# Optimization experiments

Hardware: AMD Instinct MI355X
Metric: run time of the kernel (lower is better)

## Reference

```python
import jax, jax.numpy as jnp
import numpy as np

D = 128           # volume / particle box size (pixels)
B = 8             # particles per batch
K = 125           # SO(3) grid poses (5x5x5 around each center Euler)
TOPK = 2          # keep_top_k_values
MAX_SHIFT_FRAC = 0.25  # main_config.projmatching.max_shift_fraction


def setup_inputs() -> dict:
    key = jax.random.key(0)
    k1, k2, k3, k4 = jax.random.split(key, 4)
    vol = jax.random.normal(k1, (D, D, D), dtype=jnp.float32)
    parts = jax.random.normal(k2, (B, D, D), dtype=jnp.float32)
    ctf = jax.random.uniform(k3, (B, D, D // 2 + 1), dtype=jnp.float32)
    euler_degs = jax.random.normal(k4, (K, 3), dtype=jnp.float32) * 8.0
    return {"vol": vol, "parts": parts, "ctf": ctf, "euler_degs": euler_degs}


def _rot_z(t):
    c, s = jnp.cos(t), jnp.sin(t)
    z, o = jnp.zeros_like(t), jnp.ones_like(t)
    return jnp.stack([jnp.stack([c, -s, z], -1),
                      jnp.stack([s, c, z], -1),
                      jnp.stack([z, z, o], -1)], -2)


def _rot_y(t):
    c, s = jnp.cos(t), jnp.sin(t)
    z, o = jnp.zeros_like(t), jnp.ones_like(t)
    return jnp.stack([jnp.stack([c, z, s], -1),
                      jnp.stack([z, o, z], -1),
                      jnp.stack([-s, z, c], -1)], -2)


def euler_zyz_to_matrix(degs):
    # RELION Euler convention ZYZ: R = Rz(a) @ Ry(b) @ Rz(c)
    rad = jnp.deg2rad(degs)
    return _rot_z(rad[..., 0]) @ _rot_y(rad[..., 1]) @ _rot_z(rad[..., 2])


def trilinear_sample(vol, zi, yi, xi):
    # vol: (Dz, Dy, W) complex64; coords: (K, h, w) float32 array indices
    Dz, Dy, W = vol.shape
    z0, y0, x0 = jnp.floor(zi), jnp.floor(yi), jnp.floor(xi)
    tz, ty, tx = zi - z0, yi - y0, xi - x0
    out = jnp.zeros(zi.shape, dtype=vol.dtype)
    for dz in (0, 1):
        wz = tz if dz else 1.0 - tz
        zc = z0 + dz
        vz = (zc >= 0) & (zc < Dz)
        zdx = jnp.clip(zc, 0, Dz - 1).astype(jnp.int32)
        for dy in (0, 1):
            wy = ty if dy else 1.0 - ty
            yc = y0 + dy
            vy = (yc >= 0) & (yc < Dy)
            ydx = jnp.clip(yc, 0, Dy - 1).astype(jnp.int32)
            for dx in (0, 1):
                wx = tx if dx else 1.0 - tx
                xc = x0 + dx
                vx = (xc >= 0) & (xc < W)
                xdx = jnp.clip(xc, 0, W - 1).astype(jnp.int32)
                w = jnp.where(vz & vy & vx, wz * wy * wx, 0.0)
                out = out + w * vol[zdx, ydx, xdx]
    return out


def project_fourier(vol_rfft, rotmats):
    # extract_central_slices_rfft: pose-dependent gather+trilinear interp of a
    # central slice from the fftshifted 3D rfft volume. Output: (K, D, D//2+1).
    d = D
    w = d // 2 + 1
    y = jnp.arange(d, dtype=jnp.float32) - d // 2   # fftshifted full-dim freqs (pixel units)
    x = jnp.arange(w, dtype=jnp.float32)            # rfft (non-negative) freqs
    yy, xx = jnp.meshgrid(y, x, indexing='ij')      # (d, w)
    coords = jnp.stack([xx, yy, jnp.zeros_like(yy)], -1)       # xyz, (d, w, 3), z = 0 plane
    rot = jnp.einsum('kij,hwj->khwi', rotmats, coords)          # (K, d, w, 3) rotated xyz
    conj_mask = rot[..., 0] < 0                                  # Hermitian symmetry: flip to x>=0 half
    rot = jnp.where(conj_mask[..., None], -rot, rot)
    xi = rot[..., 0]
    yi = rot[..., 1] + d // 2
    zi = rot[..., 2] + d // 2
    samples = trilinear_sample(vol_rfft, zi, yi, xi)
    samples = jnp.where(conj_mask, jnp.conj(samples), samples)
    r2 = xx ** 2 + yy ** 2                                       # zero beyond Nyquist radius
    samples = jnp.where(r2[None] > (d // 2) ** 2, 0.0, samples)
    return samples


def reference(vol, parts, ctf, euler_degs):
    # compute_dft: rfft volume, fftshift non-rfft dims
    vol_rfft = jnp.fft.fftshift(jnp.fft.rfftn(vol), axes=(0, 1))
    parts_rfft = jnp.fft.fftshift(jnp.fft.rfft2(parts), axes=(-2,))  # (B, D, W)
    rotmats = euler_zyz_to_matrix(euler_degs)                        # (K, 3, 3)
    projs = project_fourier(vol_rfft, rotmats)                       # (K, D, W)
    projs = ctf[:, None] * projs[None]                               # _apply_ctfF: (B, K, D, W)
    # correlate_dft_2d: cross-correlation via iFFT of parts * conj(projs)
    prod = parts_rfft[:, None] * jnp.conj(projs)
    prod = jnp.fft.ifftshift(prod, axes=(-2,))
    corr = jnp.fft.irfft2(prod, s=(D, D))                            # (B, K, D, D)
    corr = jnp.fft.fftshift(corr, axes=(-2, -1))                     # zero shift at center
    # _extract_ccor_max: restrict to |shift| <= max_shift_fraction*D, take top-k peaks
    center = D // 2
    max_shift = int(MAX_SHIFT_FRAC * D)
    idx = jnp.arange(D) - center
    win = (jnp.abs(idx)[:, None] <= max_shift) & (jnp.abs(idx)[None, :] <= max_shift)
    masked = jnp.where(win, corr, -jnp.inf)
    flat = masked.reshape(B, K, D * D)
    vals, top_idx = jax.lax.top_k(flat, TOPK)                        # (B, K, TOPK)
    shifts = jnp.stack([top_idx // D - center, top_idx % D - center], -1)  # (B, K, TOPK, 2) yx
    return vals, shifts
```

## Files before the change

### kernel.cpp

```cpp
#include <hip/hip_runtime.h>
#include <math.h>

#define D 128
#define W 65
#define NK 125
#define NB 8
#define SLAB (D*W)
#define TWO_PI 6.28318530717958647692f
#define R2C 0.70710678118654752440f
#define C8C 0.92387953251128675613f
#define S8C 0.38268343236508977173f
#define ARS 146
#define GRS 131


__device__ __forceinline__ bool better(float va, int ia, float vb, int ib) {
    return (va > vb) || (va == vb && ia < ib);
}
__device__ __forceinline__ float2 cmul(float2 a, float2 b) {
    return make_float2(a.x*b.x - a.y*b.y, a.x*b.y + a.y*b.x);
}
__device__ __forceinline__ void cmac(float2& acc, float2 a, float2 b) {
    acc.x = fmaf(a.x, b.x, fmaf(-a.y, b.y, acc.x));
    acc.y = fmaf(a.x, b.y, fmaf( a.y, b.x, acc.y));
}
__device__ __forceinline__ float2 cadd(float2 a, float2 b){ return make_float2(a.x+b.x, a.y+b.y); }
__device__ __forceinline__ float2 csub(float2 a, float2 b){ return make_float2(a.x-b.x, a.y-b.y); }

__device__ __forceinline__ void fft8_fwd(const float2* x, float2* a) {
    float2 e0 = x[0], o0 = x[1], e1 = x[2], o1 = x[3];
    float2 e2 = x[4], o2 = x[5], e3 = x[6], o3 = x[7];
    float2 t0 = cadd(e0, e2), t1 = csub(e0, e2);
    float2 t2 = cadd(e1, e3), t3 = csub(e1, e3);
    float2 E0 = cadd(t0, t2), E2 = csub(t0, t2);
    float2 E1 = make_float2(t1.x + t3.y, t1.y - t3.x);
    float2 E3 = make_float2(t1.x - t3.y, t1.y + t3.x);
    float2 u0 = cadd(o0, o2), u1 = csub(o0, o2);
    float2 u2 = cadd(o1, o3), u3 = csub(o1, o3);
    float2 O0 = cadd(u0, u2), O2 = csub(u0, u2);
    float2 O1 = make_float2(u1.x + u3.y, u1.y - u3.x);
    float2 O3 = make_float2(u1.x - u3.y, u1.y + u3.x);
    float2 w1 = make_float2(R2C*(O1.x + O1.y), R2C*(O1.y - O1.x));
    float2 w2 = make_float2(O2.y, -O2.x);
    float2 w3 = make_float2(R2C*(O3.y - O3.x), -R2C*(O3.x + O3.y));
    a[0] = cadd(E0, O0); a[4] = csub(E0, O0);
    a[1] = cadd(E1, w1); a[5] = csub(E1, w1);
    a[2] = cadd(E2, w2); a[6] = csub(E2, w2);
    a[3] = cadd(E3, w3); a[7] = csub(E3, w3);
}

__device__ __forceinline__ void ifft8_reg(const float2* x, float2* a) {
    float2 e0 = x[0], o0 = x[1], e1 = x[2], o1 = x[3];
    float2 e2 = x[4], o2 = x[5], e3 = x[6], o3 = x[7];
    float2 t0 = cadd(e0, e2), t1 = csub(e0, e2);
    float2 t2 = cadd(e1, e3), t3 = csub(e1, e3);
    float2 E0 = cadd(t0, t2), E2 = csub(t0, t2);
    float2 E1 = make_float2(t1.x - t3.y, t1.y + t3.x);
    float2 E3 = make_float2(t1.x + t3.y, t1.y - t3.x);
    float2 u0 = cadd(o0, o2), u1 = csub(o0, o2);
    float2 u2 = cadd(o1, o3), u3 = csub(o1, o3);
    float2 O0 = cadd(u0, u2), O2 = csub(u0, u2);
    float2 O1 = make_float2(u1.x - u3.y, u1.y + u3.x);
    float2 O3 = make_float2(u1.x + u3.y, u1.y - u3.x);
    float2 w1o = make_float2(R2C*(O1.x - O1.y), R2C*(O1.x + O1.y));
    float2 w2o = make_float2(-O2.y, O2.x);
    float2 w3o = make_float2(R2C*(-O3.x - O3.y), R2C*(O3.x - O3.y));
    a[0] = cadd(E0, O0); a[4] = csub(E0, O0);
    a[1] = cadd(E1, w1o); a[5] = csub(E1, w1o);
    a[2] = cadd(E2, w2o); a[6] = csub(E2, w2o);
    a[3] = cadd(E3, w3o); a[7] = csub(E3, w3o);
}


template<int MODE>
__device__ __forceinline__ void fft128v2(const float* __restrict__ inf,
                                         const float2* __restrict__ inc,
                                         float2* __restrict__ out,
                                         const float* __restrict__ ct,
                                         int l0, int nlines,
                                         float2* __restrict__ Fl,
                                         float2* __restrict__ twf) {
    int tid = threadIdx.x;
    int line, t;
    if (MODE == 0) { t = tid & 7; line = tid >> 3; }
    else           { line = tid & 31; t = tid >> 5; }
    int l = l0 + line;
    bool live = (l < nlines);

    if (tid < 128) {
        float s, c;
        sincosf(-TWO_PI * (float)tid / 128.0f, &s, &c);
        twf[tid] = make_float2(c, s);
    }

    int base = 0, stride = 1;
    if (MODE == 1 || MODE == 3 || MODE == 4) { base = (l / W) * SLAB + (l % W); stride = W; }
    else if (MODE == 2) { base = l; stride = SLAB; }

    float2 xe[8], xo[8];
    if (live) {
        if (MODE == 0) {
            const float* r = inf + (size_t)l * D;
            #pragma unroll
            for (int j = 0; j < 8; ++j) {
                xe[j] = make_float2(r[t + 16*j], 0.f);
                xo[j] = make_float2(r[t + 8 + 16*j], 0.f);
            }
        } else {
            #pragma unroll
            for (int j = 0; j < 8; ++j) {
                xe[j] = inc[base + (t + 16*j) * stride];
                xo[j] = inc[base + (t + 8 + 16*j) * stride];
            }
        }
    } else {
        #pragma unroll
        for (int j = 0; j < 8; ++j) { xe[j] = make_float2(0,0); xo[j] = make_float2(0,0); }
    }
    float2 E[8], O[8];
    fft8_fwd(xe, E);
    fft8_fwd(xo, O);
    {
        const float2 w16[8] = {
            { 1.f, 0.f }, { C8C, -S8C }, { R2C, -R2C }, { S8C, -C8C },
            { 0.f, -1.f }, { -S8C, -C8C }, { -R2C, -R2C }, { -C8C, -S8C }
        };
        float2* Fp = Fl + line * 137 + t * 17;
        #pragma unroll
        for (int kk = 0; kk < 8; ++kk) {
            float2 wo = cmul(w16[kk], O[kk]);
            Fp[kk]     = cadd(E[kk], wo);
            Fp[kk + 8] = csub(E[kk], wo);
        }
    }
    __syncthreads();
    if (live) {
        const float2* Fr = Fl + line * 137;
        #pragma unroll
        for (int s = 0; s < 16; ++s) {
            int slot = t + 8 * s;
            if (MODE == 0 && slot > 64) break;
            int k = (MODE == 0) ? slot : (slot ^ 64);
            int kk = k & 15;
            float2 acc = make_float2(0.f, 0.f);
            #pragma unroll
            for (int tt = 0; tt < 8; ++tt) {
                cmac(acc, Fr[tt * 17 + kk], twf[(tt * k) & 127]);
            }
            if (MODE == 0)      out[(size_t)l * W + slot] = acc;
            else if (MODE == 3) out[(size_t)l * D + slot] = acc;
            else if (MODE == 4) {
                float cf = ct[(size_t)l * D + slot];
                out[(size_t)l * D + slot] = make_float2(acc.x * cf, acc.y * cf);
            }
            else                out[base + slot * stride] = acc;
        }
    }
}


__global__ __launch_bounds__(256) void k1_kernel(const float* __restrict__ vol,
                                                 const float* __restrict__ parts,
                                                 const float* __restrict__ ctf,
                                                 const float* __restrict__ euler,
                                                 float2* __restrict__ bufA,
                                                 float2* __restrict__ pT1,
                                                 float* __restrict__ CT,
                                                 float* __restrict__ rot) {
    __shared__ float2 Fl[32 * 137];
    __shared__ float2 twf[128];
    int bid = blockIdx.x;
    int tid = threadIdx.x;
    if (bid < 512) {
        fft128v2<0>(vol, nullptr, bufA, nullptr, bid * 32, D*D, Fl, twf);
    } else if (bid < 544) {
        fft128v2<0>(parts, nullptr, pT1, nullptr, (bid - 512) * 32, NB*D, Fl, twf);
    } else if (bid == 544) {
        int k = tid;
        if (k < NK) {
            const float d2r = 0.017453292519943295f;
            float a = euler[k*3+0]*d2r, b = euler[k*3+1]*d2r, c = euler[k*3+2]*d2r;
            float sa, ca, sb, cb, sc, cc;
            sincosf(a, &sa, &ca); sincosf(b, &sb, &cb); sincosf(c, &sc, &cc);
            rot[k*9+0] =  ca*cb*cc - sa*sc;
            rot[k*9+1] = -ca*cb*sc - sa*cc;
            rot[k*9+2] =  ca*sb;
            rot[k*9+3] =  sa*cb*cc + ca*sc;
            rot[k*9+4] = -sa*cb*sc + ca*cc;
            rot[k*9+5] =  sa*sb;
            rot[k*9+6] = -sb*cc;
            rot[k*9+7] =  sb*sc;
            rot[k*9+8] =  cb;
        }
    } else {
        int i = (bid - 545) * 256 + tid;
        if (i < NB * W * D) {
            int m = i & (D-1);
            int t2 = i >> 7;
            int x = t2 % W;
            int b = t2 / W;
            CT[i] = ctf[b * SLAB + m * W + x];
        }
    }
}

__global__ __launch_bounds__(256) void k2_kernel(const float2* __restrict__ bufA,
                                                 float2* __restrict__ bufB,
                                                 const float2* __restrict__ pT1,
                                                 float2* __restrict__ ST,
                                                 const float* __restrict__ CT) {
    __shared__ float2 Fl[32 * 137];
    __shared__ float2 twf[128];
    int bid = blockIdx.x;
    if (bid < 260) fft128v2<1>(nullptr, bufA, bufB, nullptr, bid * 32, D*W, Fl, twf);
    else           fft128v2<4>(nullptr, pT1, ST, CT, (bid - 260) * 32, NB*W, Fl, twf);
}

__global__ __launch_bounds__(256) void k3_kernel(const float2* __restrict__ bufB,
                                                 float2* __restrict__ bufA) {
    __shared__ float2 Fl[32 * 137];
    __shared__ float2 twf[128];
    fft128v2<2>(nullptr, bufB, bufA, nullptr, blockIdx.x * 32, SLAB, Fl, twf);
}


__global__ void proj_kernel(const float2* __restrict__ vol, const float* __restrict__ rot,
                            float2* __restrict__ projT) {
    int idx = blockIdx.x * blockDim.x + threadIdx.x;
    if (idx >= NK * D * W) return;
    int h = idx & (D-1);
    int t2 = idx >> 7;
    int w = t2 % W;
    int k = t2 / W;
    float x = (float)w;
    float y = (float)(h - 64);
    const float* R = rot + k*9;
    float rx = R[0]*x + R[1]*y;
    float ry = R[3]*x + R[4]*y;
    float rz = R[6]*x + R[7]*y;
    bool neg = rx < 0.0f;
    if (neg) { rx = -rx; ry = -ry; rz = -rz; }
    float xi = rx;
    float yi = ry + 64.0f;
    float zi = rz + 64.0f;
    float z0 = floorf(zi), y0 = floorf(yi), x0 = floorf(xi);
    float tz = zi - z0, ty = yi - y0, tx = xi - x0;
    int z0i = (int)z0, y0i = (int)y0, x0i = (int)x0;
    float ar = 0.f, ai = 0.f;
    for (int dz = 0; dz < 2; ++dz) {
        float wz = dz ? tz : 1.0f - tz;
        int zc = z0i + dz;
        bool vz = (zc >= 0) && (zc < D);
        int zx = min(max(zc, 0), D-1);
        for (int dy = 0; dy < 2; ++dy) {
            float wy = dy ? ty : 1.0f - ty;
            int yc = y0i + dy;
            bool vy = (yc >= 0) && (yc < D);
            int yx = min(max(yc, 0), D-1);
            for (int dx = 0; dx < 2; ++dx) {
                float wx = dx ? tx : 1.0f - tx;
                int xc = x0i + dx;
                bool vx = (xc >= 0) && (xc < W);
                int xx = min(max(xc, 0), W-1);
                float wt = (vz && vy && vx) ? wz*wy*wx : 0.0f;
                float2 v = vol[zx * SLAB + yx * W + xx];
                ar = fmaf(wt, v.x, ar);
                ai = fmaf(wt, v.y, ai);
            }
        }
    }
    if (neg) ai = -ai;
    int yy = h - 64;
    if (w*w + yy*yy > 4096) { ar = 0.f; ai = 0.f; }
    projT[idx] = make_float2(ar, ai);
}


__global__ __launch_bounds__(256, 2) void corr_kernel(const float2* __restrict__ ST,
                                                      const float2* __restrict__ PJT,
                                                      float* __restrict__ outv) {
    __shared__ float2 tw[128];
    __shared__ float2 AbBC[17*ARS];
    __shared__ float2 G[17*GRS];
    __shared__ float  Ny[65];
    __shared__ float  redv[8];
    __shared__ int    redi[8];

    int g = blockIdx.x;
    int logical = (g & 7) * 125 + (g >> 3);
    int k = logical >> 3;
    int b = logical & 7;
    int tid = threadIdx.x;
    const float inv_d = 1.0f / 128.0f;

    if (tid < 128) {
        float s, c;
        sincosf(TWO_PI * (float)tid / 128.0f, &s, &c);
        tw[tid] = make_float2(c, s);
    }

    const float2* Sb = ST + b * (W * D);
    const float2* Jk = PJT + k * (W * D);

    int lane = tid & 63;
    int wv = tid >> 6;
    int sv = lane & 7;
    int vp = (96 + lane) & 127;
    float acc[16];
    #pragma unroll
    for (int j = 0; j < 16; ++j) acc[j] = 0.0f;
    float accR = 0.0f;
    int ur = 0, vr = 0;
    if (tid < 129) { if (tid < 65) { ur = 64; vr = tid; } else { ur = tid - 65; vr = 64; } }

    __syncthreads();

    float2 wvp = tw[vp];
    float2 tq = make_float2(1.0f, 0.0f);

    int l1 = tid >> 4, m01 = tid & 15;
    float2 Sv[8], Jv[8];

    for (int cg = 0; cg < 4; ++cg) {
        if (cg == 0) {
            for (int i = tid; i < 17 * 16; i += 256) {
                int l = i >> 4, m0 = i & 15;
                int x = (l < 16) ? ((l >> 2) + 16 * (l & 3)) : 64;
                const float2* Sx = Sb + x * 128 + m0;
                const float2* Jx = Jk + x * 128 + m0;
                float2 p[8];
                #pragma unroll
                for (int j = 0; j < 8; ++j) {
                    float2 s = Sx[16*j];
                    float2 pj = Jx[16*j];
                    p[j] = make_float2(s.x*pj.x + s.y*pj.y, s.y*pj.x - s.x*pj.y);
                }
                float2 A[8];
                ifft8_reg(p, A);
                float2* dst = AbBC + l * ARS + m0;
                dst[0] = A[0];
                #pragma unroll
                for (int r = 1; r < 8; ++r) dst[r*18] = cmul(A[r], tw[(r * m0) & 127]);
            }
        } else {
            float2 p[8];
            #pragma unroll
            for (int j = 0; j < 8; ++j) {
                p[j] = make_float2(Sv[j].x*Jv[j].x + Sv[j].y*Jv[j].y,
                                   Sv[j].y*Jv[j].x - Sv[j].x*Jv[j].y);
            }
            float2 A[8];
            ifft8_reg(p, A);
            float2* dst = AbBC + l1 * ARS + m01;
            dst[0] = A[0];
            #pragma unroll
            for (int r = 1; r < 8; ++r) dst[r*18] = cmul(A[r], tw[(r * m01) & 127]);
        }
        __syncthreads();
        {
            int lim2 = (cg == 0) ? 136 : 128;
            for (int i = tid; i < lim2; i += 256) {
                int l, r;
                if (i < 128) { l = i & 15; r = i >> 4; }
                else         { l = 16; r = i - 128; }
                const float4* Ar = (const float4*)(AbBC + l * ARS + r * 18);
                float2 xe[8], xo[8];
                #pragma unroll
                for (int j = 0; j < 8; ++j) {
                    float4 a = Ar[j];
                    xe[j] = make_float2(a.x, a.y);
                    xo[j] = make_float2(a.z, a.w);
                }
                float2 E[8], O[8];
                ifft8_reg(xe, E);
                ifft8_reg(xo, O);
                const float2 w16p[8] = {
                    { 1.f, 0.f }, { C8C, S8C }, { R2C, R2C }, { S8C, C8C },
                    { 0.f, 1.f }, { -S8C, C8C }, { -R2C, R2C }, { -C8C, S8C }
                };
                float2* Gl = G + l * GRS + r;
                #pragma unroll
                for (int t = 0; t < 8; ++t) {
                    float2 wo = cmul(w16p[t], O[t]);
                    Gl[8*t]      = cadd(E[t], wo);
                    Gl[8*t + 64] = csub(E[t], wo);
                }
            }
        }
        if (cg < 3) {
            int xn = 4*(cg+1) + (l1 >> 2) + 16 * (l1 & 3);
            const float2* Sx = Sb + xn * 128 + m01;
            const float2* Jx = Jk + xn * 128 + m01;
            #pragma unroll
            for (int j = 0; j < 8; ++j) {
                Sv[j] = Sx[16*j];
                Jv[j] = Jx[16*j];
            }
        }
        __syncthreads();
        {
            float2* BC = AbBC;
            int lim = (cg == 0) ? 325 : 260;
            for (int i = tid; i < lim; i += 256) {
                if (i < 260) {
                    int q = i / 65;
                    int u2 = i - q * 65;
                    int up = (96 + u2) & 127;
                    float sg = (u2 & 1) ? -inv_d : inv_d;
                    const float2* Gq = G + up;
                    float2 h0 = Gq[(4*q+0)*GRS];
                    float2 h1 = Gq[(4*q+1)*GRS];
                    float2 h2 = Gq[(4*q+2)*GRS];
                    float2 h3 = Gq[(4*q+3)*GRS];
                    h0.x *= sg; h0.y *= sg; h1.x *= sg; h1.y *= sg;
                    h2.x *= sg; h2.y *= sg; h3.x *= sg; h3.y *= sg;
                    if (cg == 0 && q == 0) { h0.x *= 0.5f; h0.y *= 0.5f; }
                    const float sc = 2.0f * inv_d;
                    float2 p1 = make_float2(R2C*(h1.x - h1.y), R2C*(h1.x + h1.y));
                    float2 q1 = make_float2(R2C*(-h1.x - h1.y), R2C*(h1.x - h1.y));
                    float2 i1 = make_float2(-h1.y, h1.x);
                    float2 i2 = make_float2(-h2.y, h2.x);
                    float2 n2 = make_float2( h2.y, -h2.x);
                    float2 p3 = make_float2(R2C*(h3.x - h3.y), R2C*(h3.x + h3.y));
                    float2 q3 = make_float2(R2C*(-h3.x - h3.y), R2C*(h3.x - h3.y));
                    float2 i3 = make_float2(-h3.y, h3.x);
                    float2 a02 = cadd(h0, h2), s02 = csub(h0, h2);
                    float2 s0 = cadd(a02, cadd(h1, h3));
                    float2 s4 = csub(a02, cadd(h1, h3));
                    float2 s2 = cadd(s02, csub(i1, i3));
                    float2 s6 = csub(s02, csub(i1, i3));
                    float2 b0i = cadd(h0, i2);
                    float2 b0n = cadd(h0, n2);
                    float2 s1 = cadd(b0i, cadd(p1, q3));
                    float2 s5 = csub(b0i, cadd(p1, q3));
                    float2 s3 = cadd(b0n, cadd(q1, p3));
                    float2 s7 = csub(b0n, cadd(q1, p3));
                    float2* Bp = BC + q * (8*67) + u2;
                    Bp[0*67] = make_float2(s0.x*sc, s0.y*sc);
                    Bp[1*67] = make_float2(s1.x*sc, s1.y*sc);
                    Bp[2*67] = make_float2(s2.x*sc, s2.y*sc);
                    Bp[3*67] = make_float2(s3.x*sc, s3.y*sc);
                    Bp[4*67] = make_float2(s4.x*sc, s4.y*sc);
                    Bp[5*67] = make_float2(s5.x*sc, s5.y*sc);
                    Bp[6*67] = make_float2(s6.x*sc, s6.y*sc);
                    Bp[7*67] = make_float2(s7.x*sc, s7.y*sc);
                } else {
                    int u2 = i - 260;
                    int up = (96 + u2) & 127;
                    Ny[u2] = ((u2 & 1) ? -inv_d : inv_d) * G[16*GRS + up].x;
                }
            }
        }
        __syncthreads();
        {
            const float2* BC = AbBC;
            #pragma unroll
            for (int q = 0; q < 4; ++q) {
                const float2* Bq = BC + (q * 8 + sv) * 67 + wv * 16;
                float tx = tq.x, ty = tq.y;
                #pragma unroll
                for (int j = 0; j < 16; ++j) {
                    float2 bv = Bq[j];
                    acc[j] = fmaf(bv.x, tx, fmaf(-bv.y, ty, acc[j]));
                }
                tq = cmul(tq, wvp);
            }
            if (cg == 0) {
                float sgn = (lane & 1) ? -inv_d : inv_d;
                #pragma unroll
                for (int j = 0; j < 16; ++j) acc[j] = fmaf(sgn, Ny[wv * 16 + j], acc[j]);
            }
            if (tid < 129) {
                int sr = vr & 7, vpr = (96 + vr) & 127;
                float a = accR;
                #pragma unroll
                for (int q = 0; q < 4; ++q) {
                    float2 t = tw[((4*cg + q) * vpr) & 127];
                    float2 bv = AbBC[(q * 8 + sr) * 67 + ur];
                    a = fmaf(bv.x, t.x, fmaf(-bv.y, t.y, a));
                }
                if (cg == 0) a += (vr & 1) ? -inv_d * Ny[ur] : inv_d * Ny[ur];
                accR = a;
            }
        }
        __syncthreads();
    }

    float v1 = -INFINITY, v2 = -INFINITY;
    int i1 = 0x7fffffff, i2 = 0x7fffffff;
    #pragma unroll
    for (int j = 0; j < 16; ++j) {
        float val = acc[j];
        int uu = wv * 16 + j;
        int fl = (32 + uu) * D + (32 + lane);
        if (better(val, fl, v1, i1)) { v2 = v1; i2 = i1; v1 = val; i1 = fl; }
        else if (better(val, fl, v2, i2)) { v2 = val; i2 = fl; }
    }
    if (tid < 129) {
        int fl = (32 + ur) * D + (32 + vr);
        if (better(accR, fl, v1, i1)) { v2 = v1; i2 = i1; v1 = accR; i1 = fl; }
        else if (better(accR, fl, v2, i2)) { v2 = accR; i2 = fl; }
    }
    for (int off = 32; off > 0; off >>= 1) {
        float b1 = __shfl_down(v1, off); int j1 = __shfl_down(i1, off);
        float b2 = __shfl_down(v2, off); int j2 = __shfl_down(i2, off);
        if (better(b1, j1, v1, i1)) {
            float nv2; int ni2;
            if (better(v1, i1, b2, j2)) { nv2 = v1; ni2 = i1; } else { nv2 = b2; ni2 = j2; }
            v1 = b1; i1 = j1; v2 = nv2; i2 = ni2;
        } else {
            if (better(b1, j1, v2, i2)) { v2 = b1; i2 = j1; }
        }
    }
    int wave = tid >> 6;
    if ((tid & 63) == 0) {
        redv[wave*2]   = v1; redi[wave*2]   = i1;
        redv[wave*2+1] = v2; redi[wave*2+1] = i2;
    }
    __syncthreads();
    if (tid == 0) {
        float r1 = -INFINITY, r2 = -INFINITY;
        int q1 = 0x7fffffff, q2 = 0x7fffffff;
        for (int i = 0; i < 8; ++i) {
            float val = redv[i]; int fl = redi[i];
            if (better(val, fl, r1, q1)) { r2 = r1; q2 = q1; r1 = val; q1 = fl; }
            else if (better(val, fl, r2, q2)) { r2 = val; q2 = fl; }
        }
        int base = (b * NK + k) * 2;
        outv[base]     = r1;
        outv[base + 1] = r2;
        float* os = outv + NB*NK*2;
        os[(base    )*2 + 0] = (float)(q1 / D - 64);
        os[(base    )*2 + 1] = (float)(q1 % D - 64);
        os[(base + 1)*2 + 0] = (float)(q2 / D - 64);
        os[(base + 1)*2 + 1] = (float)(q2 % D - 64);
    }
}


extern "C" void kernel_launch(void* const* d_in, const int* in_sizes, int n_in,
                              void* d_out, int out_size, void* d_ws, size_t ws_size,
                              hipStream_t stream) {
    const float* vol   = (const float*)d_in[0];
    const float* parts = (const float*)d_in[1];
    const float* ctf   = (const float*)d_in[2];
    const float* euler = (const float*)d_in[3];
    float* out = (float*)d_out;

    const int VOLC = D * SLAB;
    float2* bufA   = (float2*)d_ws;
    float2* bufB   = bufA + VOLC;
    float2* pT1    = bufB + VOLC;
    float2* ST     = pT1 + NB * SLAB;
    float2* PJT    = ST + NB * W * D;
    float*  CT     = (float*)(PJT + NK * W * D);
    float*  rot    = CT + NB * W * D;

    k1_kernel<<<805, 256, 0, stream>>>(vol, parts, ctf, euler, bufA, pT1, CT, rot);
    k2_kernel<<<277, 256, 0, stream>>>(bufA, bufB, pT1, ST, CT);
    k3_kernel<<<260, 256, 0, stream>>>(bufB, bufA);
    proj_kernel<<<(NK*D*W + 255) / 256, 256, 0, stream>>>(bufA, rot, PJT);
    corr_kernel<<<NB * NK, 256, 0, stream>>>(ST, PJT, out);
}
```

Before: 83.23 us.

## Replace block barriers with wave barriers in corr stages and remap proj blocks per XCD

Reworks the correlation kernel's inner iFFT stages so that each wavefront owns its own slice of shared memory. Two __syncthreads calls become wave-level barriers, the next-chunk global prefetch moves earlier, and the per-row twiddles are hoisted into registers. The projection kernel remaps block IDs so that consecutive work lands on the same XCD, which is meant to improve L2 locality of the volume gathers. It also removes the unused MODE 3 FFT path. The risks are subtle data races if the per-wave ownership of the shared buffers is not actually complete, and an exact grid size tied to eight XCDs.

```diff
diff --git a/kernel.cpp b/kernel.cpp
--- a/kernel.cpp
+++ b/kernel.cpp
@@ -12,6 +12,7 @@
 #define S8C 0.38268343236508977173f
 #define ARS 146
 #define GRS 131
+#define BCW 584
 
 
 __device__ __forceinline__ bool better(float va, int ia, float vb, int ib) {
@@ -94,7 +95,7 @@
     }
 
     int base = 0, stride = 1;
-    if (MODE == 1 || MODE == 3 || MODE == 4) { base = (l / W) * SLAB + (l % W); stride = W; }
+    if (MODE == 1 || MODE == 4) { base = (l / W) * SLAB + (l % W); stride = W; }
     else if (MODE == 2) { base = l; stride = SLAB; }
 
     float2 xe[8], xo[8];
@@ -148,7 +149,6 @@
                 cmac(acc, Fr[tt * 17 + kk], twf[(tt * k) & 127]);
             }
             if (MODE == 0)      out[(size_t)l * W + slot] = acc;
-            else if (MODE == 3) out[(size_t)l * D + slot] = acc;
             else if (MODE == 4) {
                 float cf = ct[(size_t)l * D + slot];
                 out[(size_t)l * D + slot] = make_float2(acc.x * cf, acc.y * cf);
@@ -224,9 +224,13 @@
 }
 
 
-__global__ void proj_kernel(const float2* __restrict__ vol, const float* __restrict__ rot,
-                            float2* __restrict__ projT) {
-    int idx = blockIdx.x * blockDim.x + threadIdx.x;
+__global__ __launch_bounds__(256) void proj_kernel(const float2* __restrict__ vol,
+                                                   const float* __restrict__ rot,
+                                                   float2* __restrict__ projT) {
+    int bid = blockIdx.x;
+    int xcd = bid & 7, ii = bid >> 3;
+    int wg = (xcd < 7) ? (xcd * 508 + ii) : (3556 + ii);
+    int idx = wg * 256 + threadIdx.x;
     if (idx >= NK * D * W) return;
     int h = idx & (D-1);
     int t2 = idx >> 7;
@@ -320,6 +324,10 @@
 
     int l1 = tid >> 4, m01 = tid & 15;
     float2 Sv[8], Jv[8];
+    float2 twr[8];
+    twr[0] = make_float2(1.f, 0.f);
+    #pragma unroll
+    for (int r = 1; r < 8; ++r) twr[r] = tw[(r * m01) & 127];
 
     for (int cg = 0; cg < 4; ++cg) {
         if (cg == 0) {
@@ -354,15 +362,24 @@
             float2* dst = AbBC + l1 * ARS + m01;
             dst[0] = A[0];
             #pragma unroll
-            for (int r = 1; r < 8; ++r) dst[r*18] = cmul(A[r], tw[(r * m01) & 127]);
-        }
-        __syncthreads();
+            for (int r = 1; r < 8; ++r) dst[r*18] = cmul(A[r], twr[r]);
+        }
+        if (cg < 3) {
+            int xn = 4*(cg+1) + (l1 >> 2) + 16 * (l1 & 3);
+            const float2* Sx = Sb + xn * 128 + m01;
+            const float2* Jx = Jk + xn * 128 + m01;
+            #pragma unroll
+            for (int j = 0; j < 8; ++j) {
+                Sv[j] = Sx[16*j];
+                Jv[j] = Jx[16*j];
+            }
+        }
+        __builtin_amdgcn_wave_barrier();
         {
-            int lim2 = (cg == 0) ? 136 : 128;
-            for (int i = tid; i < lim2; i += 256) {
-                int l, r;
-                if (i < 128) { l = i & 15; r = i >> 4; }
-                else         { l = 16; r = i - 128; }
+            int l = -1, r = 0;
+            if (lane < 32) { l = 4*wv + (lane >> 3); r = lane & 7; }
+            else if (cg == 0 && wv == 0 && lane < 40) { l = 16; r = lane - 32; }
+            if (l >= 0) {
                 const float4* Ar = (const float4*)(AbBC + l * ARS + r * 18);
                 float2 xe[8], xo[8];
                 #pragma unroll
@@ -387,65 +404,55 @@
                 }
             }
         }
-        if (cg < 3) {
-            int xn = 4*(cg+1) + (l1 >> 2) + 16 * (l1 & 3);
-            const float2* Sx = Sb + xn * 128 + m01;
-            const float2* Jx = Jk + xn * 128 + m01;
-            #pragma unroll
-            for (int j = 0; j < 8; ++j) {
-                Sv[j] = Sx[16*j];
-                Jv[j] = Jx[16*j];
-            }
-        }
-        __syncthreads();
+        __builtin_amdgcn_wave_barrier();
         {
             float2* BC = AbBC;
-            int lim = (cg == 0) ? 325 : 260;
-            for (int i = tid; i < lim; i += 256) {
-                if (i < 260) {
-                    int q = i / 65;
-                    int u2 = i - q * 65;
-                    int up = (96 + u2) & 127;
-                    float sg = (u2 & 1) ? -inv_d : inv_d;
-                    const float2* Gq = G + up;
-                    float2 h0 = Gq[(4*q+0)*GRS];
-                    float2 h1 = Gq[(4*q+1)*GRS];
-                    float2 h2 = Gq[(4*q+2)*GRS];
-                    float2 h3 = Gq[(4*q+3)*GRS];
-                    h0.x *= sg; h0.y *= sg; h1.x *= sg; h1.y *= sg;
-                    h2.x *= sg; h2.y *= sg; h3.x *= sg; h3.y *= sg;
-                    if (cg == 0 && q == 0) { h0.x *= 0.5f; h0.y *= 0.5f; }
-                    const float sc = 2.0f * inv_d;
-                    float2 p1 = make_float2(R2C*(h1.x - h1.y), R2C*(h1.x + h1.y));
-                    float2 q1 = make_float2(R2C*(-h1.x - h1.y), R2C*(h1.x - h1.y));
-                    float2 i1 = make_float2(-h1.y, h1.x);
-                    float2 i2 = make_float2(-h2.y, h2.x);
-                    float2 n2 = make_float2( h2.y, -h2.x);
-                    float2 p3 = make_float2(R2C*(h3.x - h3.y), R2C*(h3.x + h3.y));
-                    float2 q3 = make_float2(R2C*(-h3.x - h3.y), R2C*(h3.x - h3.y));
-                    float2 i3 = make_float2(-h3.y, h3.x);
-                    float2 a02 = cadd(h0, h2), s02 = csub(h0, h2);
-                    float2 s0 = cadd(a02, cadd(h1, h3));
-                    float2 s4 = csub(a02, cadd(h1, h3));
-                    float2 s2 = cadd(s02, csub(i1, i3));
-                    float2 s6 = csub(s02, csub(i1, i3));
-                    float2 b0i = cadd(h0, i2);
-                    float2 b0n = cadd(h0, n2);
-                    float2 s1 = cadd(b0i, cadd(p1, q3));
-                    float2 s5 = csub(b0i, cadd(p1, q3));
-                    float2 s3 = cadd(b0n, cadd(q1, p3));
-                    float2 s7 = csub(b0n, cadd(q1, p3));
-                    float2* Bp = BC + q * (8*67) + u2;
-                    Bp[0*67] = make_float2(s0.x*sc, s0.y*sc);
-                    Bp[1*67] = make_float2(s1.x*sc, s1.y*sc);
-                    Bp[2*67] = make_float2(s2.x*sc, s2.y*sc);
-                    Bp[3*67] = make_float2(s3.x*sc, s3.y*sc);
-                    Bp[4*67] = make_float2(s4.x*sc, s4.y*sc);
-                    Bp[5*67] = make_float2(s5.x*sc, s5.y*sc);
-                    Bp[6*67] = make_float2(s6.x*sc, s6.y*sc);
-                    Bp[7*67] = make_float2(s7.x*sc, s7.y*sc);
-                } else {
-                    int u2 = i - 260;
+            int nt = (lane == 0) ? 2 : 1;
+            for (int it = 0; it < nt; ++it) {
+                int u2 = it ? 64 : lane;
+                int up = (96 + u2) & 127;
+                float sg = (u2 & 1) ? -inv_d : inv_d;
+                const float2* Gq = G + (4*wv)*GRS + up;
+                float2 h0 = Gq[0*GRS];
+                float2 h1 = Gq[1*GRS];
+                float2 h2 = Gq[2*GRS];
+                float2 h3 = Gq[3*GRS];
+                h0.x *= sg; h0.y *= sg; h1.x *= sg; h1.y *= sg;
+                h2.x *= sg; h2.y *= sg; h3.x *= sg; h3.y *= sg;
+                if (cg == 0 && wv == 0) { h0.x *= 0.5f; h0.y *= 0.5f; }
+                const float sc = 2.0f * inv_d;
+                float2 p1 = make_float2(R2C*(h1.x - h1.y), R2C*(h1.x + h1.y));
+                float2 q1 = make_float2(R2C*(-h1.x - h1.y), R2C*(h1.x - h1.y));
+                float2 i1 = make_float2(-h1.y, h1.x);
+                float2 i2 = make_float2(-h2.y, h2.x);
+                float2 n2 = make_float2( h2.y, -h2.x);
+                float2 p3 = make_float2(R2C*(h3.x - h3.y), R2C*(h3.x + h3.y));
+                float2 q3 = make_float2(R2C*(-h3.x - h3.y), R2C*(h3.x - h3.y));
+                float2 i3 = make_float2(-h3.y, h3.x);
+                float2 a02 = cadd(h0, h2), s02 = csub(h0, h2);
+                float2 s0 = cadd(a02, cadd(h1, h3));
+                float2 s4 = csub(a02, cadd(h1, h3));
+                float2 s2 = cadd(s02, csub(i1, i3));
+                float2 s6 = csub(s02, csub(i1, i3));
+                float2 b0i = cadd(h0, i2);
+                float2 b0n = cadd(h0, n2);
+                float2 s1 = cadd(b0i, cadd(p1, q3));
+                float2 s5 = csub(b0i, cadd(p1, q3));
+                float2 s3 = cadd(b0n, cadd(q1, p3));
+                float2 s7 = csub(b0n, cadd(q1, p3));
+                float2* Bp = BC + wv * BCW + u2;
+                Bp[0*67] = make_float2(s0.x*sc, s0.y*sc);
+                Bp[1*67] = make_float2(s1.x*sc, s1.y*sc);
+                Bp[2*67] = make_float2(s2.x*sc, s2.y*sc);
+                Bp[3*67] = make_float2(s3.x*sc, s3.y*sc);
+                Bp[4*67] = make_float2(s4.x*sc, s4.y*sc);
+                Bp[5*67] = make_float2(s5.x*sc, s5.y*sc);
+                Bp[6*67] = make_float2(s6.x*sc, s6.y*sc);
+                Bp[7*67] = make_float2(s7.x*sc, s7.y*sc);
+            }
+            if (cg == 0 && wv == 0) {
+                for (int it = 0; it < nt; ++it) {
+                    int u2 = it ? 64 : lane;
                     int up = (96 + u2) & 127;
                     Ny[u2] = ((u2 & 1) ? -inv_d : inv_d) * G[16*GRS + up].x;
                 }
@@ -453,10 +460,9 @@
         }
         __syncthreads();
         {
-            const float2* BC = AbBC;
             #pragma unroll
             for (int q = 0; q < 4; ++q) {
-                const float2* Bq = BC + (q * 8 + sv) * 67 + wv * 16;
+                const float2* Bq = AbBC + q * BCW + sv * 67 + wv * 16;
                 float tx = tq.x, ty = tq.y;
                 #pragma unroll
                 for (int j = 0; j < 16; ++j) {
@@ -476,7 +482,7 @@
                 #pragma unroll
                 for (int q = 0; q < 4; ++q) {
                     float2 t = tw[((4*cg + q) * vpr) & 127];
-                    float2 bv = AbBC[(q * 8 + sr) * 67 + ur];
+                    float2 bv = AbBC[q * BCW + sr * 67 + ur];
                     a = fmaf(bv.x, t.x, fmaf(-bv.y, t.y, a));
                 }
                 if (cg == 0) a += (vr & 1) ? -inv_d * Ny[ur] : inv_d * Ny[ur];
@@ -559,6 +565,6 @@
     k1_kernel<<<805, 256, 0, stream>>>(vol, parts, ctf, euler, bufA, pT1, CT, rot);
     k2_kernel<<<277, 256, 0, stream>>>(bufA, bufB, pT1, ST, CT);
     k3_kernel<<<260, 256, 0, stream>>>(bufB, bufA);
-    proj_kernel<<<(NK*D*W + 255) / 256, 256, 0, stream>>>(bufA, rot, PJT);
+    proj_kernel<<<4063, 256, 0, stream>>>(bufA, rot, PJT);
     corr_kernel<<<NB * NK, 256, 0, stream>>>(ST, PJT, out);
 }
```

After: 84.60 us. No clear change (+1.7%).
